# Kernel tuning notes

Hardware: AMD Instinct MI355X
Metric: run time of the kernel (lower is better)

Reference implementation:

```python
import jax, jax.numpy as jnp
import numpy as np

K_TOP = 1  # k_top in the source module


def setup_inputs() -> dict:
    key = jax.random.key(0)
    k1, k2 = jax.random.split(key)
    n_frames, dim = 8192, 1024  # n_frames_max, WavLM layer-6 feature dim
    return {
        "source_features": jax.random.normal(k1, (n_frames, dim), dtype=jnp.float32),
        "target_features": jax.random.normal(k2, (n_frames, dim), dtype=jnp.float32),
    }


def reference(source_features, target_features):
    # fast_cosine_dist: 1 - cosine_similarity, via normalized GEMM
    eps = 1e-12
    sn = source_features / jnp.maximum(
        jnp.linalg.norm(source_features, axis=-1, keepdims=True), eps)
    tn = target_features / jnp.maximum(
        jnp.linalg.norm(target_features, axis=-1, keepdims=True), eps)
    dists = 1.0 - jnp.einsum("sd,td->st", sn, tn)  # [n_src, n_tgt]
    # topk(k=K_TOP, largest=False): take top-k of negated distances
    _, idx = jax.lax.top_k(-dists, K_TOP)  # [n_src, K_TOP]
    # gather matched target frames and average over the k neighbors
    linear_target = target_features[idx].mean(axis=1)  # [n_src, dim]
    return linear_target
```

## Files before the change

kernel.cpp:

```cpp
#include <hip/hip_runtime.h>
#include <math.h>

#define DIM      1024
#define NSTRIPES 16
#define PAD      4
#define MAXSLOTS 32
#define EPS      0.08f

typedef __attribute__((ext_vector_type(8))) __bf16 bf16x8;
typedef __attribute__((ext_vector_type(4))) __bf16 bf16x4;
typedef __attribute__((ext_vector_type(4))) float f32x4;

#define FENCE() asm volatile("" ::: "memory")

__device__ __forceinline__ void async16(void* lds, const void* g) {
    __builtin_amdgcn_global_load_lds(
        (const __attribute__((address_space(1))) unsigned int*)g,
        (__attribute__((address_space(3))) unsigned int*)lds, 16, 0, 0);
}

__global__ void convert_all_kernel(const float* __restrict__ src,
                                   const float* __restrict__ tgt,
                                   unsigned short* __restrict__ bfA,
                                   unsigned short* __restrict__ bfB,
                                   float* __restrict__ inv_t, int M, int N) {
    int row = blockIdx.x * 4 + (threadIdx.x >> 6);
    int l = threadIdx.x & 63;
    if (row < M) {
        const float4* rp = (const float4*)(src + (size_t)row * DIM);
        unsigned short* wp = bfA + (size_t)row * DIM;
#pragma unroll
        for (int p = 0; p < 2; ++p) {
            int c = l + 64 * p;
            float4 v0 = rp[2 * c], v1 = rp[2 * c + 1];
            bf16x8 o;
            o[0] = (__bf16)v0.x; o[1] = (__bf16)v0.y;
            o[2] = (__bf16)v0.z; o[3] = (__bf16)v0.w;
            o[4] = (__bf16)v1.x; o[5] = (__bf16)v1.y;
            o[6] = (__bf16)v1.z; o[7] = (__bf16)v1.w;
            *(bf16x8*)(wp + (size_t)c * 8) = o;
        }
        return;
    }
    int trow = row - M;
    if (trow >= N) return;
    const float4* rp = (const float4*)(tgt + (size_t)trow * DIM);
    unsigned short* wp = bfB + (size_t)trow * DIM;
    float ss = 0.f;
#pragma unroll
    for (int p = 0; p < 4; ++p) {
        float4 v = rp[l + 64 * p];
        bf16x4 o;
        o[0] = (__bf16)v.x; o[1] = (__bf16)v.y;
        o[2] = (__bf16)v.z; o[3] = (__bf16)v.w;
        *(bf16x4*)(wp + (size_t)(l + 64 * p) * 4) = o;
        ss = fmaf(v.x, v.x, ss);
        ss = fmaf(v.y, v.y, ss);
        ss = fmaf(v.z, v.z, ss);
        ss = fmaf(v.w, v.w, ss);
    }
#pragma unroll
    for (int off = 32; off; off >>= 1) ss += __shfl_xor(ss, off, 64);
    if (l == 0) inv_t[trow] = 1.0f / fmaxf(sqrtf(ss), 1e-12f);
}

__global__ __launch_bounds__(512) void mfma_argmax256_kernel(
    const unsigned short* __restrict__ Abf,
    const unsigned short* __restrict__ Bbf,
    const float* __restrict__ inv_t,
    float* __restrict__ sbest,
    int M, int N) {
    __shared__ __align__(16) unsigned short sA[2][16384];
    __shared__ __align__(16) unsigned short sB[2][16384];
    const int tid = threadIdx.x;
    const int w = tid >> 6, l = tid & 63;
    const int wr = w >> 2, wc = w & 3;
    int bx = blockIdx.x, by = blockIdx.y;
    {
        int gx = gridDim.x;
        int nwg = gx * gridDim.y;
        if ((nwg & 7) == 0) {
            int lin = bx + gx * by;
            int swz = (lin & 7) * (nwg >> 3) + (lin >> 3);
            bx = swz % gx;
            by = swz / gx;
        }
    }
    const int rowBase = bx * 256;
    const int colBase = by * 256;
    const int ngroups = N >> 3;
    const int NT = DIM / 64;

    int goff[4], lbase[4];
#pragma unroll
    for (int j = 0; j < 4; ++j) {
        int c = j * 512 + tid;
        int row = c >> 3, c8 = c & 7;
        goff[j] = row * DIM + (c8 ^ (row & 7)) * 8;
        lbase[j] = (j * 512 + w * 64) * 8;
    }

    const int q = l >> 4;
    int aoff[8], boff[4];
#pragma unroll
    for (int m = 0; m < 8; ++m) {
        int row = wr * 128 + m * 16 + (l & 15);
        aoff[m] = (row * 128 + q * 16) ^ ((row & 7) << 4);
    }
#pragma unroll
    for (int n = 0; n < 4; ++n) {
        int col = wc * 64 + n * 16 + (l & 15);
        boff[n] = (col * 128 + q * 16) ^ ((col & 7) << 4);
    }

    f32x4 acc[8][4];
#pragma unroll
    for (int m = 0; m < 8; ++m)
#pragma unroll
        for (int n = 0; n < 4; ++n) acc[m][n] = (f32x4){0.f, 0.f, 0.f, 0.f};

    const unsigned short* ga = Abf + (size_t)rowBase * DIM;
    const unsigned short* gb = Bbf + (size_t)colBase * DIM;

    auto stage = [&](int t) {
        unsigned short* dA = &sA[t & 1][0];
        unsigned short* dB = &sB[t & 1][0];
#pragma unroll
        for (int j = 0; j < 4; ++j) {
            async16(dA + lbase[j], ga + t * 64 + goff[j]);
            async16(dB + lbase[j], gb + t * 64 + goff[j]);
        }
    };
    auto compute = [&](int i) {
        const char* bA = (const char*)&sA[i & 1][0];
        const char* bB = (const char*)&sB[i & 1][0];
#pragma unroll
        for (int s = 0; s < 2; ++s) {
            bf16x8 af[8], bfr[4];
#pragma unroll
            for (int m = 0; m < 8; ++m)
                af[m] = *(const bf16x8*)(bA + (aoff[m] ^ (s << 6)));
#pragma unroll
            for (int n = 0; n < 4; ++n)
                bfr[n] = *(const bf16x8*)(bB + (boff[n] ^ (s << 6)));
            __builtin_amdgcn_s_setprio(1);
#pragma unroll
            for (int m = 0; m < 8; ++m)
#pragma unroll
                for (int n = 0; n < 4; ++n)
                    acc[m][n] = __builtin_amdgcn_mfma_f32_16x16x32_bf16(
                        bfr[n], af[m], acc[m][n], 0, 0, 0);
            __builtin_amdgcn_s_setprio(0);
        }
    };

    stage(0);
    for (int i = 0; i < NT - 1; ++i) {
        stage(i + 1);
        asm volatile("s_waitcnt vmcnt(8)" ::: "memory");
        FENCE(); __builtin_amdgcn_s_barrier(); FENCE();
        compute(i);
        FENCE(); __builtin_amdgcn_s_barrier(); FENCE();
    }
    asm volatile("s_waitcnt vmcnt(0)" ::: "memory");
    FENCE(); __builtin_amdgcn_s_barrier(); FENCE();
    compute(NT - 1);

#pragma unroll
    for (int n = 0; n < 4; ++n) {
        float4 it4 = *(const float4*)&inv_t[colBase + wc * 64 + n * 16 + (q << 2)];
#pragma unroll
        for (int m = 0; m < 8; ++m) {
            float v = acc[m][n][0] * it4.x;
            v = fmaxf(v, acc[m][n][1] * it4.y);
            v = fmaxf(v, acc[m][n][2] * it4.z);
            v = fmaxf(v, acc[m][n][3] * it4.w);
            v = fmaxf(v, __shfl_xor(v, 16, 64));
            if ((l & 16) == 0) {
                int row = rowBase + wr * 128 + m * 16 + (l & 15);
                int g = (colBase >> 3) + wc * 8 + n * 2 + (q >> 1);
                sbest[(size_t)row * ngroups + g] = v;
            }
        }
    }
}

__global__ __launch_bounds__(256) void flag_refine_kernel(
    const float* __restrict__ sbest, const float* __restrict__ src,
    const float* __restrict__ tgt, const float* __restrict__ inv_t,
    float* __restrict__ out, int ngroups, int gsh) {
    __shared__ __align__(16) float4 s_src[256];
    __shared__ float wmax[4];
    __shared__ int s_slots[MAXSLOTS];
    __shared__ int s_cnt;
    __shared__ float s_wv[4];
    __shared__ int s_wi[4];
    __shared__ int s_best;
    const int row = blockIdx.x;
    const int tid = threadIdx.x;
    const int w = tid >> 6, l = tid & 63;
    const int GW = 1 << gsh;

    s_src[tid] = ((const float4*)(src + (size_t)row * DIM))[tid];
    if (tid == 0) s_cnt = 0;

    const float* p = sbest + (size_t)row * ngroups;
    const int nper = ngroups >> 8;
    float v[4];
    float mx = -1e30f;
    for (int j = 0; j < nper; ++j) {
        v[j] = p[tid + j * 256];
        mx = fmaxf(mx, v[j]);
    }
#pragma unroll
    for (int off = 32; off; off >>= 1) mx = fmaxf(mx, __shfl_xor(mx, off, 64));
    if (l == 0) wmax[w] = mx;
    __syncthreads();
    float thr = fmaxf(fmaxf(wmax[0], wmax[1]), fmaxf(wmax[2], wmax[3])) - EPS;
    for (int j = 0; j < nper; ++j) {
        if (v[j] >= thr) {
            int s = atomicAdd(&s_cnt, 1);
            if (s < MAXSLOTS) s_slots[s] = tid + j * 256;
        }
    }
    __syncthreads();

    int m = s_cnt;
    if (m > MAXSLOTS) m = MAXSLOTS;
    const int ncand = m << gsh;
    const int grp = tid >> 4;
    const int ln = tid & 15;
    float bv = -1e30f;
    int bi = 0x7fffffff;
    for (int c = grp; c < ncand; c += 16) {
        int col = (s_slots[c >> gsh] << gsh) + (c & (GW - 1));
        const float4* trow = (const float4*)(tgt + (size_t)col * DIM);
        float dot = 0.f;
#pragma unroll
        for (int j = 0; j < 16; ++j) {
            float4 a = s_src[ln + 16 * j];
            float4 b = trow[ln + 16 * j];
            dot = fmaf(a.x, b.x, dot);
            dot = fmaf(a.y, b.y, dot);
            dot = fmaf(a.z, b.z, dot);
            dot = fmaf(a.w, b.w, dot);
        }
        dot += __shfl_xor(dot, 1, 64);
        dot += __shfl_xor(dot, 2, 64);
        dot += __shfl_xor(dot, 4, 64);
        dot += __shfl_xor(dot, 8, 64);
        float vv = dot * inv_t[col];
        if (vv > bv || (vv == bv && col < bi)) { bv = vv; bi = col; }
    }
#pragma unroll
    for (int off = 16; off <= 32; off <<= 1) {
        float v2 = __shfl_xor(bv, off, 64);
        int i2 = __shfl_xor(bi, off, 64);
        if (v2 > bv || (v2 == bv && i2 < bi)) { bv = v2; bi = i2; }
    }
    if (l == 0) { s_wv[w] = bv; s_wi[w] = bi; }
    __syncthreads();
    if (tid == 0) {
        float vv = s_wv[0];
        int ix = s_wi[0];
#pragma unroll
        for (int t = 1; t < 4; ++t) {
            float v2 = s_wv[t];
            int i2 = s_wi[t];
            if (v2 > vv || (v2 == vv && i2 < ix)) { vv = v2; ix = i2; }
        }
        s_best = ix;
    }
    __syncthreads();
    int ixb = s_best;
    ((float4*)(out + (size_t)row * DIM))[tid] =
        ((const float4*)(tgt + (size_t)ixb * DIM))[tid];
}

__global__ void inv_norm_kernel(const float* __restrict__ t,
                                float* __restrict__ inv_t, int n) {
    int wave = (int)((blockIdx.x * blockDim.x + threadIdx.x) >> 6);
    int lane = threadIdx.x & 63;
    if (wave >= n) return;
    const float4* row = (const float4*)(t + (size_t)wave * DIM);
    float ss = 0.f;
#pragma unroll
    for (int p = 0; p < 4; ++p) {
        float4 v = row[lane + 64 * p];
        ss = fmaf(v.x, v.x, ss);
        ss = fmaf(v.y, v.y, ss);
        ss = fmaf(v.z, v.z, ss);
        ss = fmaf(v.w, v.w, ss);
    }
#pragma unroll
    for (int off = 32; off; off >>= 1) ss += __shfl_xor(ss, off, 64);
    if (lane == 0) inv_t[wave] = 1.0f / fmaxf(sqrtf(ss), 1e-12f);
}

__global__ __launch_bounds__(256) void fused_argmax_kernel(
    const float* __restrict__ A, const float* __restrict__ B,
    const float* __restrict__ inv_t, float* __restrict__ sbest,
    int* __restrict__ sidx, int M, int N) {
    __shared__ __align__(16) float sA[32][128 + PAD];
    __shared__ __align__(16) float sB[32][128 + PAD];
    const int tid = threadIdx.x;
    const int tx = tid & 15;
    const int ty = tid >> 4;
    const int rowBase = blockIdx.x * 128;
    const int stripe = blockIdx.y;
    const int stripeN = N / NSTRIPES;
    const int colBase0 = stripe * stripeN;
    const int lr = tid >> 3;
    const int lk = (tid & 7) << 2;
    float best[8];
    int bidx[8];
#pragma unroll
    for (int i = 0; i < 8; ++i) { best[i] = -1e30f; bidx[i] = 0; }
    for (int nt = 0; nt < stripeN / 128; ++nt) {
        const int colBase = colBase0 + nt * 128;
        float acc[8][8];
#pragma unroll
        for (int i = 0; i < 8; ++i)
#pragma unroll
            for (int j = 0; j < 8; ++j) acc[i][j] = 0.f;
        for (int kt = 0; kt < DIM / 32; ++kt) {
            const int k0 = kt * 32;
            __syncthreads();
#pragma unroll
            for (int p = 0; p < 4; ++p) {
                int r = lr + 32 * p;
                float4 va = *(const float4*)(A + (size_t)(rowBase + r) * DIM + k0 + lk);
                sA[lk + 0][r] = va.x; sA[lk + 1][r] = va.y;
                sA[lk + 2][r] = va.z; sA[lk + 3][r] = va.w;
                float4 vb = *(const float4*)(B + (size_t)(colBase + r) * DIM + k0 + lk);
                sB[lk + 0][r] = vb.x; sB[lk + 1][r] = vb.y;
                sB[lk + 2][r] = vb.z; sB[lk + 3][r] = vb.w;
            }
            __syncthreads();
#pragma unroll 4
            for (int k = 0; k < 32; ++k) {
                float4 af0 = *(const float4*)&sA[k][ty * 8];
                float4 af1 = *(const float4*)&sA[k][ty * 8 + 4];
                float4 bf0 = *(const float4*)&sB[k][tx * 8];
                float4 bf1 = *(const float4*)&sB[k][tx * 8 + 4];
                float a[8] = {af0.x, af0.y, af0.z, af0.w, af1.x, af1.y, af1.z, af1.w};
                float b[8] = {bf0.x, bf0.y, bf0.z, bf0.w, bf1.x, bf1.y, bf1.z, bf1.w};
#pragma unroll
                for (int i = 0; i < 8; ++i)
#pragma unroll
                    for (int j = 0; j < 8; ++j)
                        acc[i][j] = fmaf(a[i], b[j], acc[i][j]);
            }
        }
#pragma unroll
        for (int j = 0; j < 8; ++j) {
            int col = colBase + tx * 8 + j;
            float it = inv_t[col];
#pragma unroll
            for (int i = 0; i < 8; ++i) {
                float s = acc[i][j] * it;
                if (s > best[i]) { best[i] = s; bidx[i] = col; }
            }
        }
    }
#pragma unroll
    for (int i = 0; i < 8; ++i) {
        float v = best[i];
        int ix = bidx[i];
#pragma unroll
        for (int off = 1; off < 16; off <<= 1) {
            float v2 = __shfl_xor(v, off, 64);
            int ix2 = __shfl_xor(ix, off, 64);
            if (v2 > v || (v2 == v && ix2 < ix)) { v = v2; ix = ix2; }
        }
        if (tx == 0) {
            int row = rowBase + ty * 8 + i;
            sbest[(size_t)stripe * M + row] = v;
            sidx[(size_t)stripe * M + row] = ix;
        }
    }
}

__global__ void gather_kernel(const float* __restrict__ B,
                              const float* __restrict__ sbest,
                              const int* __restrict__ sidx,
                              float* __restrict__ out, int M) {
    int row = blockIdx.x;
    float v = -1e30f;
    int ix = 0;
#pragma unroll
    for (int s = 0; s < NSTRIPES; ++s) {
        float v2 = sbest[(size_t)s * M + row];
        int ix2 = sidx[(size_t)s * M + row];
        if (v2 > v || (v2 == v && ix2 < ix)) { v = v2; ix = ix2; }
    }
    const float4* srcp = (const float4*)(B + (size_t)ix * DIM);
    float4* dstp = (float4*)(out + (size_t)row * DIM);
    dstp[threadIdx.x] = srcp[threadIdx.x];
}

extern "C" void kernel_launch(void* const* d_in, const int* in_sizes, int n_in,
                              void* d_out, int out_size, void* d_ws, size_t ws_size,
                              hipStream_t stream) {
    const float* src = (const float*)d_in[0];
    const float* tgt = (const float*)d_in[1];
    float* out = (float*)d_out;
    int M = in_sizes[0] / DIM;
    int N = in_sizes[1] / DIM;

    auto align256 = [](size_t x) { return (x + 255) & ~(size_t)255; };
    size_t sz_invt = align256((size_t)N * 4);
    size_t sz_bfA = align256((size_t)M * DIM * 2);
    size_t sz_bfB = align256((size_t)N * DIM * 2);
    size_t common = sz_invt + sz_bfA + sz_bfB;
    size_t sz_sbest8 = align256((size_t)M * (N / 8) * 4);

    if ((M % 256) == 0 && (N % 2048) == 0 && N / 8 <= 1024 &&
        ws_size >= common + sz_sbest8) {
        char* p = (char*)d_ws;
        float* inv_t = (float*)p;                 p += sz_invt;
        unsigned short* bfA = (unsigned short*)p; p += sz_bfA;
        unsigned short* bfB = (unsigned short*)p; p += sz_bfB;
        float* sbest = (float*)p;
        int ngroups = N >> 3;

        convert_all_kernel<<<dim3((M + N + 3) / 4), 256, 0, stream>>>(
            src, tgt, bfA, bfB, inv_t, M, N);
        mfma_argmax256_kernel<<<dim3(M / 256, N / 256), 512, 0, stream>>>(
            bfA, bfB, inv_t, sbest, M, N);
        flag_refine_kernel<<<dim3(M), 256, 0, stream>>>(
            sbest, src, tgt, inv_t, out, ngroups, 3);
    } else {
        char* ws = (char*)d_ws;
        float* sbest = (float*)ws;
        int* sidx = (int*)(ws + (size_t)NSTRIPES * M * sizeof(float));
        float* inv_t = (float*)(ws + (size_t)NSTRIPES * M * (sizeof(float) + sizeof(int)));
        inv_norm_kernel<<<dim3((N + 3) / 4), 256, 0, stream>>>(tgt, inv_t, N);
        fused_argmax_kernel<<<dim3(M / 128, NSTRIPES), 256, 0, stream>>>(
            src, tgt, inv_t, sbest, sidx, M, N);
        gather_kernel<<<dim3(M), 256, 0, stream>>>(tgt, sbest, sidx, out, M);
    }
}
```

Measured before the change: 230.9 us.

## Refine one source row per wave and drop GEMM workgroup swizzle

The refine kernel now gives each wavefront one source row instead of a whole 256-thread block per row. This removes the block-wide syncs and the cross-wave reductions, and reads the group maxima as float4. Each wave evaluates its candidate columns four at a time instead of sixteen, which lowers per-row parallelism but lets four rows run per block. Separately, the GEMM kernel drops its XCD-aware block-index swizzle and uses plain blockIdx mapping, which may change L2 locality on the multi-die MI355X.

```diff
diff --git a/kernel.cpp b/kernel.cpp
--- a/kernel.cpp
+++ b/kernel.cpp
@@ -75,19 +75,8 @@
     const int tid = threadIdx.x;
     const int w = tid >> 6, l = tid & 63;
     const int wr = w >> 2, wc = w & 3;
-    int bx = blockIdx.x, by = blockIdx.y;
-    {
-        int gx = gridDim.x;
-        int nwg = gx * gridDim.y;
-        if ((nwg & 7) == 0) {
-            int lin = bx + gx * by;
-            int swz = (lin & 7) * (nwg >> 3) + (lin >> 3);
-            bx = swz % gx;
-            by = swz / gx;
-        }
-    }
-    const int rowBase = bx * 256;
-    const int colBase = by * 256;
+    const int rowBase = blockIdx.x * 256;
+    const int colBase = blockIdx.y * 256;
     const int ngroups = N >> 3;
     const int NT = DIM / 64;
 
@@ -185,60 +174,56 @@
     }
 }
 
-__global__ __launch_bounds__(256) void flag_refine_kernel(
+__global__ __launch_bounds__(256) void flag_refine_wave_kernel(
     const float* __restrict__ sbest, const float* __restrict__ src,
     const float* __restrict__ tgt, const float* __restrict__ inv_t,
     float* __restrict__ out, int ngroups, int gsh) {
-    __shared__ __align__(16) float4 s_src[256];
-    __shared__ float wmax[4];
-    __shared__ int s_slots[MAXSLOTS];
-    __shared__ int s_cnt;
-    __shared__ float s_wv[4];
-    __shared__ int s_wi[4];
-    __shared__ int s_best;
-    const int row = blockIdx.x;
-    const int tid = threadIdx.x;
-    const int w = tid >> 6, l = tid & 63;
+    __shared__ __align__(16) float4 s_src[4][256];
+    __shared__ int s_slots[4][MAXSLOTS];
+    __shared__ int s_cnt[4];
+    const int wv = threadIdx.x >> 6;
+    const int l = threadIdx.x & 63;
+    const int row = blockIdx.x * 4 + wv;
     const int GW = 1 << gsh;
 
-    s_src[tid] = ((const float4*)(src + (size_t)row * DIM))[tid];
-    if (tid == 0) s_cnt = 0;
-
-    const float* p = sbest + (size_t)row * ngroups;
-    const int nper = ngroups >> 8;
-    float v[4];
+    const float4* srow = (const float4*)(src + (size_t)row * DIM);
+#pragma unroll
+    for (int j = 0; j < 4; ++j) s_src[wv][l + 64 * j] = srow[l + 64 * j];
+    if (l == 0) s_cnt[wv] = 0;
+    __syncthreads();
+
+    const float4* p4 = (const float4*)(sbest + (size_t)row * ngroups);
+    const int nj = ngroups >> 8;
+    float4 g[4];
     float mx = -1e30f;
-    for (int j = 0; j < nper; ++j) {
-        v[j] = p[tid + j * 256];
-        mx = fmaxf(mx, v[j]);
+    for (int j = 0; j < nj; ++j) {
+        g[j] = p4[l + 64 * j];
+        mx = fmaxf(mx, fmaxf(fmaxf(g[j].x, g[j].y), fmaxf(g[j].z, g[j].w)));
     }
 #pragma unroll
     for (int off = 32; off; off >>= 1) mx = fmaxf(mx, __shfl_xor(mx, off, 64));
-    if (l == 0) wmax[w] = mx;
-    __syncthreads();
-    float thr = fmaxf(fmaxf(wmax[0], wmax[1]), fmaxf(wmax[2], wmax[3])) - EPS;
-    for (int j = 0; j < nper; ++j) {
-        if (v[j] >= thr) {
-            int s = atomicAdd(&s_cnt, 1);
-            if (s < MAXSLOTS) s_slots[s] = tid + j * 256;
-        }
-    }
-    __syncthreads();
-
-    int m = s_cnt;
+    float thr = mx - EPS;
+    for (int j = 0; j < nj; ++j) {
+        int gbase = (l + 64 * j) << 2;
+        if (g[j].x >= thr) { int s = atomicAdd(&s_cnt[wv], 1); if (s < MAXSLOTS) s_slots[wv][s] = gbase; }
+        if (g[j].y >= thr) { int s = atomicAdd(&s_cnt[wv], 1); if (s < MAXSLOTS) s_slots[wv][s] = gbase + 1; }
+        if (g[j].z >= thr) { int s = atomicAdd(&s_cnt[wv], 1); if (s < MAXSLOTS) s_slots[wv][s] = gbase + 2; }
+        if (g[j].w >= thr) { int s = atomicAdd(&s_cnt[wv], 1); if (s < MAXSLOTS) s_slots[wv][s] = gbase + 3; }
+    }
+    int m = s_cnt[wv];
     if (m > MAXSLOTS) m = MAXSLOTS;
     const int ncand = m << gsh;
-    const int grp = tid >> 4;
-    const int ln = tid & 15;
+    const int grp = l >> 4;
+    const int ln = l & 15;
     float bv = -1e30f;
     int bi = 0x7fffffff;
-    for (int c = grp; c < ncand; c += 16) {
-        int col = (s_slots[c >> gsh] << gsh) + (c & (GW - 1));
+    for (int c = grp; c < ncand; c += 4) {
+        int col = (s_slots[wv][c >> gsh] << gsh) + (c & (GW - 1));
         const float4* trow = (const float4*)(tgt + (size_t)col * DIM);
         float dot = 0.f;
 #pragma unroll
         for (int j = 0; j < 16; ++j) {
-            float4 a = s_src[ln + 16 * j];
+            float4 a = s_src[wv][ln + 16 * j];
             float4 b = trow[ln + 16 * j];
             dot = fmaf(a.x, b.x, dot);
             dot = fmaf(a.y, b.y, dot);
@@ -258,23 +243,10 @@
         int i2 = __shfl_xor(bi, off, 64);
         if (v2 > bv || (v2 == bv && i2 < bi)) { bv = v2; bi = i2; }
     }
-    if (l == 0) { s_wv[w] = bv; s_wi[w] = bi; }
-    __syncthreads();
-    if (tid == 0) {
-        float vv = s_wv[0];
-        int ix = s_wi[0];
-#pragma unroll
-        for (int t = 1; t < 4; ++t) {
-            float v2 = s_wv[t];
-            int i2 = s_wi[t];
-            if (v2 > vv || (v2 == vv && i2 < ix)) { vv = v2; ix = i2; }
-        }
-        s_best = ix;
-    }
-    __syncthreads();
-    int ixb = s_best;
-    ((float4*)(out + (size_t)row * DIM))[tid] =
-        ((const float4*)(tgt + (size_t)ixb * DIM))[tid];
+    const float4* win = (const float4*)(tgt + (size_t)bi * DIM);
+    float4* dst = (float4*)(out + (size_t)row * DIM);
+#pragma unroll
+    for (int j = 0; j < 4; ++j) dst[l + 64 * j] = win[l + 64 * j];
 }
 
 __global__ void inv_norm_kernel(const float* __restrict__ t,
@@ -428,7 +400,7 @@
             src, tgt, bfA, bfB, inv_t, M, N);
         mfma_argmax256_kernel<<<dim3(M / 256, N / 256), 512, 0, stream>>>(
             bfA, bfB, inv_t, sbest, M, N);
-        flag_refine_kernel<<<dim3(M), 256, 0, stream>>>(
+        flag_refine_wave_kernel<<<dim3(M / 4), 256, 0, stream>>>(
             sbest, src, tgt, inv_t, out, ngroups, 3);
     } else {
         char* ws = (char*)d_ws;
```

Measured after the change: 236.6 us. 1.02x slower.
